# Kernel optimization log

Hardware: AMD Instinct MI355X
Metric: run time of the kernel (lower is better)

Reference implementation:

```python
import jax, jax.numpy as jnp
import numpy as np

B, N, DIM = 4, 2048, 512
HEADS, DIM_HEAD = 8, 64
HID = HEADS * DIM_HEAD


def setup_inputs() -> dict:
    key = jax.random.key(0)
    k1, k2, k3, k4, k5 = jax.random.split(key, 5)
    x = jax.random.normal(k1, (B, N, DIM), jnp.float32)
    pos_bias = jax.random.normal(k2, (HEADS, N, N), jnp.float32) * 0.02
    focus_present_mask = jax.random.bernoulli(k3, 0.5, (B,))
    w_qkv = jax.random.normal(k4, (DIM, 3 * HID), jnp.float32) * (DIM ** -0.5)
    w_out = jax.random.normal(k5, (HID, DIM), jnp.float32) * (HID ** -0.5)
    return {"x": x, "pos_bias": pos_bias, "focus_present_mask": focus_present_mask,
            "w_qkv": w_qkv, "w_out": w_out}


def reference(x, pos_bias, focus_present_mask, w_qkv, w_out):
    scale = DIM_HEAD ** -0.5
    qkv = x @ w_qkv                                   # (B, N, 3*HID)
    q, k, v = jnp.split(qkv, 3, axis=-1)

    def to_heads(t):  # (B, N, HID) -> (B, H, N, D)
        return t.reshape(B, N, HEADS, DIM_HEAD).transpose(0, 2, 1, 3)

    q = to_heads(q) * scale
    k = to_heads(k)
    v = to_heads(v)

    sim = jnp.einsum('bhid,bhjd->bhij', q, k) + pos_bias[None]  # (B, H, N, N)

    # focus_present_mask[b] True -> attend only to self (eye); False -> attend all
    eye = jnp.eye(N, dtype=bool)
    mask = jnp.where(focus_present_mask[:, None, None, None],
                     eye[None, None], jnp.bool_(True))          # (B,1,N,N)
    sim = jnp.where(mask, sim, -jnp.finfo(sim.dtype).max)

    attn = jax.nn.softmax(sim, axis=-1)  # stable softmax == subtract-max + softmax
    out = jnp.einsum('bhij,bhjd->bhid', attn, v)
    out = out.transpose(0, 2, 1, 3).reshape(B, N, HID)
    return out @ w_out
```

## Files before the change

kernel.cpp:

```cpp
#include <hip/hip_runtime.h>
#include <hip/hip_bf16.h>
#include <float.h>

#define B_   4
#define N_   2048
#define DIM_ 512
#define H_   8
#define DH_  64

typedef unsigned short ushort;
typedef __attribute__((ext_vector_type(8))) short short8;
typedef __attribute__((ext_vector_type(4))) float f32x4;

__device__ __forceinline__ ushort f2bf(float f) {
    union { float f; unsigned u; } v; v.f = f;
    return (ushort)((v.u + 0x7fffu + ((v.u >> 16) & 1u)) >> 16);
}
__device__ __forceinline__ float bf2f(ushort u) {
    union { unsigned u; float f; } v; v.u = ((unsigned)u) << 16;
    return v.f;
}

typedef const __attribute__((address_space(1))) unsigned int* gas_t;
typedef __attribute__((address_space(3))) unsigned int* las_t;
__device__ __forceinline__ void gl_lds16(const void* g, void* l) {
    __builtin_amdgcn_global_load_lds((gas_t)g, (las_t)l, 16, 0, 0);
}

__global__ __launch_bounds__(256) void prep_kernel(
    const float* __restrict__ x, const float* __restrict__ wqkv,
    const float* __restrict__ wo,
    ushort* __restrict__ xb, ushort* __restrict__ wqkvT, ushort* __restrict__ woT)
{
    __shared__ ushort tile[64][72];
    const int bx = blockIdx.x;
    const int t = threadIdx.x;
    if (bx < 2048) {
        int gid = bx * 256 + t;
        const float4* xv = (const float4*)x;
        float4 v0 = xv[gid * 2], v1 = xv[gid * 2 + 1];
        uint4 pk;
        pk.x = (unsigned)f2bf(v0.x) | ((unsigned)f2bf(v0.y) << 16);
        pk.y = (unsigned)f2bf(v0.z) | ((unsigned)f2bf(v0.w) << 16);
        pk.z = (unsigned)f2bf(v1.x) | ((unsigned)f2bf(v1.y) << 16);
        pk.w = (unsigned)f2bf(v1.z) | ((unsigned)f2bf(v1.w) << 16);
        ((uint4*)xb)[gid] = pk;
        return;
    }
    int bi = bx - 2048;
    const float* src; ushort* dst; int C, tc, tr;
    if (bi < 192) { src = wqkv; dst = wqkvT; C = 1536; tc = bi % 24; tr = bi / 24; }
    else { bi -= 192; src = wo; dst = woT; C = 512; tc = bi & 7; tr = bi >> 3; }

    const int row = t >> 2, c16 = (t & 3) * 16;
    const float* sp = src + (size_t)(tr * 64 + row) * C + tc * 64 + c16;
    #pragma unroll
    for (int i = 0; i < 4; ++i) {
        float4 v = ((const float4*)sp)[i];
        tile[row][c16 + i * 4 + 0] = f2bf(v.x);
        tile[row][c16 + i * 4 + 1] = f2bf(v.y);
        tile[row][c16 + i * 4 + 2] = f2bf(v.z);
        tile[row][c16 + i * 4 + 3] = f2bf(v.w);
    }
    __syncthreads();
    ushort s[16];
    #pragma unroll
    for (int i = 0; i < 16; ++i) s[i] = tile[c16 + i][row];
    ushort* dp = dst + (size_t)(tc * 64 + row) * 512 + tr * 64 + c16;
    *(uint4*)dp       = *(uint4*)&s[0];
    *(uint4*)(dp + 8) = *(uint4*)&s[8];
}

__global__ __launch_bounds__(256) void vtrans_kernel(
    const ushort* __restrict__ v, ushort* __restrict__ vT)
{
    __shared__ ushort tile[64][72];
    const int nt = blockIdx.x, bh = blockIdx.y;
    const int t = threadIdx.x;
    const int row = t >> 2, c16 = (t & 3) * 16;
    const ushort* src = v + ((size_t)bh * 2048 + nt * 64 + row) * 64 + c16;
    *(uint4*)&tile[row][c16]     = *(const uint4*)src;
    *(uint4*)&tile[row][c16 + 8] = *(const uint4*)(src + 8);
    __syncthreads();
    ushort s[16];
    #pragma unroll
    for (int i = 0; i < 16; ++i) s[i] = tile[c16 + i][row];
    ushort* dst = vT + ((size_t)bh * 64 + row) * 2048 + nt * 64 + c16;
    *(uint4*)dst       = *(uint4*)&s[0];
    *(uint4*)(dst + 8) = *(uint4*)&s[8];
}

__global__ __launch_bounds__(256) void qkv_gemm(
    const ushort* __restrict__ A, const ushort* __restrict__ Bt,
    ushort* __restrict__ qb, ushort* __restrict__ kb, ushort* __restrict__ vb)
{
    __shared__ ushort sA[128 * 64];
    __shared__ ushort sB[128 * 64];
    const int bn = blockIdx.x;
    const int bm = blockIdx.y;
    const int t = threadIdx.x, w_id = t >> 6, lane = t & 63;
    const int l15 = lane & 15, quad = lane >> 4;
    const int mo = (w_id & 1) * 64, no = (w_id >> 1) * 64;
    const int lr = lane >> 3, lc = (lane & 7) * 8;

    f32x4 acc[4][4] = {};

    for (int kt = 0; kt < 8; ++kt) {
        __syncthreads();
        #pragma unroll
        for (int i = 0; i < 4; ++i) {
            int j = w_id * 4 + i;
            gl_lds16(A  + (size_t)(bm * 128 + j * 8 + lr) * 512 + kt * 64 + lc, &sA[j * 512]);
            gl_lds16(Bt + (size_t)(bn * 128 + j * 8 + lr) * 512 + kt * 64 + lc, &sB[j * 512]);
        }
        __syncthreads();
        #pragma unroll
        for (int c = 0; c < 2; ++c) {
            short8 af[4], bf[4];
            #pragma unroll
            for (int mt = 0; mt < 4; ++mt)
                af[mt] = *(const short8*)&sA[(mo + mt * 16 + l15) * 64 + c * 32 + quad * 8];
            #pragma unroll
            for (int n2 = 0; n2 < 4; ++n2)
                bf[n2] = *(const short8*)&sB[(no + n2 * 16 + l15) * 64 + c * 32 + quad * 8];
            #pragma unroll
            for (int mt = 0; mt < 4; ++mt)
                #pragma unroll
                for (int n2 = 0; n2 < 4; ++n2)
                    acc[mt][n2] = __builtin_amdgcn_mfma_f32_16x16x32_bf16(af[mt], bf[n2], acc[mt][n2], 0, 0, 0);
        }
    }

    const int gn0 = bn * 128 + no;
    const int which = gn0 >> 9;
    const int h = (gn0 >> 6) & 7;
    ushort* dst = which == 0 ? qb : (which == 1 ? kb : vb);
    const float sc = which == 0 ? 0.125f : 1.0f;
    #pragma unroll
    for (int mt = 0; mt < 4; ++mt) {
        const int m0 = bm * 128 + mo + mt * 16 + quad * 4;
        #pragma unroll
        for (int n2 = 0; n2 < 4; ++n2) {
            int d = n2 * 16 + l15;
            #pragma unroll
            for (int r = 0; r < 4; ++r) {
                int m = m0 + r, b = m >> 11, n = m & 2047;
                dst[((size_t)(b * 8 + h) * 2048 + n) * 64 + d] = f2bf(acc[mt][n2][r] * sc);
            }
        }
    }
}

__global__ __launch_bounds__(256) void attn_kernel(
    const ushort* __restrict__ qg, const ushort* __restrict__ kg,
    const ushort* __restrict__ vTg, const float* __restrict__ bias,
    const int* __restrict__ mask,
    ushort* __restrict__ po, float* __restrict__ pl)
{
    const int bid = blockIdx.x;
    const int qblk = bid & 31, s = (bid >> 5) & 1, h = (bid >> 6) & 7, b = bid >> 9;
    if (mask[b] != 0) return;

    const int t = threadIdx.x, w_id = t >> 6, lane = t & 63;
    const int l15 = lane & 15, quad = lane >> 4;
    const int lr = lane >> 3, lc = (lane & 7) * 8;
    const int bh = b * 8 + h;
    const int kbase = s * 1024;

    __shared__ ushort lds_k[64 * 64];
    __shared__ ushort lds_vt[64 * 64];
    __shared__ ushort lds_sp[4 * 16 * 68];

    const ushort* kptr = kg  + (size_t)bh * 2048 * 64;
    const ushort* vtp  = vTg + (size_t)bh * 64 * 2048;

    const ushort* qrp = qg + (size_t)bh * 2048 * 64 + (size_t)(qblk * 64 + w_id * 16 + l15) * 64;
    short8 qf0 = *(const short8*)(qrp + quad * 8);
    short8 qf1 = *(const short8*)(qrp + 32 + quad * 8);

    const int qrow0 = qblk * 64 + w_id * 16 + quad * 4;
    const float* bp = bias + ((size_t)h * 2048 + qrow0) * 2048 + kbase;

    float breg[16];
    #pragma unroll
    for (int tt = 0; tt < 4; ++tt)
        #pragma unroll
        for (int r = 0; r < 4; ++r)
            breg[tt * 4 + r] = bp[(size_t)r * 2048 + tt * 16 + l15];

    f32x4 o[4] = {};
    float lsum[4] = {0.f, 0.f, 0.f, 0.f};

    for (int it = 0; it < 16; ++it) {
        __syncthreads();
        #pragma unroll
        for (int i = 0; i < 2; ++i) {
            int j = w_id * 2 + i;
            gl_lds16(kptr + (size_t)(kbase + it * 64 + j * 8 + lr) * 64 + lc, &lds_k[j * 512]);
            gl_lds16(vtp + (size_t)(j * 8 + lr) * 2048 + kbase + it * 64 + lc, &lds_vt[j * 512]);
        }
        __syncthreads();

        f32x4 sv[4] = {};
        #pragma unroll
        for (int tt = 0; tt < 4; ++tt) {
            short8 kf0 = *(const short8*)&lds_k[(tt * 16 + l15) * 64 + quad * 8];
            short8 kf1 = *(const short8*)&lds_k[(tt * 16 + l15) * 64 + 32 + quad * 8];
            sv[tt] = __builtin_amdgcn_mfma_f32_16x16x32_bf16(qf0, kf0, sv[tt], 0, 0, 0);
            sv[tt] = __builtin_amdgcn_mfma_f32_16x16x32_bf16(qf1, kf1, sv[tt], 0, 0, 0);
        }
        #pragma unroll
        for (int tt = 0; tt < 4; ++tt)
            #pragma unroll
            for (int r = 0; r < 4; ++r)
                sv[tt][r] += breg[tt * 4 + r];

        if (it < 15) {
            #pragma unroll
            for (int tt = 0; tt < 4; ++tt)
                #pragma unroll
                for (int r = 0; r < 4; ++r)
                    breg[tt * 4 + r] = bp[(size_t)r * 2048 + (it + 1) * 64 + tt * 16 + l15];
        }

        const int prow0 = (w_id * 16 + quad * 4) * 68;
        #pragma unroll
        for (int r = 0; r < 4; ++r) {
            float e0 = __expf(sv[0][r]), e1 = __expf(sv[1][r]);
            float e2 = __expf(sv[2][r]), e3 = __expf(sv[3][r]);
            lsum[r] += (e0 + e1) + (e2 + e3);
            const int pr = prow0 + r * 68;
            lds_sp[pr + l15]      = f2bf(e0);
            lds_sp[pr + 16 + l15] = f2bf(e1);
            lds_sp[pr + 32 + l15] = f2bf(e2);
            lds_sp[pr + 48 + l15] = f2bf(e3);
        }

        asm volatile("s_waitcnt lgkmcnt(0)" ::: "memory");

        short8 pf0 = *(const short8*)&lds_sp[(w_id * 16 + l15) * 68 + quad * 8];
        short8 pf1 = *(const short8*)&lds_sp[(w_id * 16 + l15) * 68 + 32 + quad * 8];
        #pragma unroll
        for (int nt = 0; nt < 4; ++nt) {
            short8 vf0 = *(const short8*)&lds_vt[(nt * 16 + l15) * 64 + quad * 8];
            short8 vf1 = *(const short8*)&lds_vt[(nt * 16 + l15) * 64 + 32 + quad * 8];
            o[nt] = __builtin_amdgcn_mfma_f32_16x16x32_bf16(pf0, vf0, o[nt], 0, 0, 0);
            o[nt] = __builtin_amdgcn_mfma_f32_16x16x32_bf16(pf1, vf1, o[nt], 0, 0, 0);
        }
    }

    #pragma unroll
    for (int r = 0; r < 4; ++r) {
        #pragma unroll
        for (int off = 1; off < 16; off <<= 1)
            lsum[r] += __shfl_xor(lsum[r], off, 64);
    }

    #pragma unroll
    for (int r = 0; r < 4; ++r) {
        const int qrow = qrow0 + r;
        const size_t base = ((size_t)(s * 32 + bh) * 2048 + qrow) * 64;
        #pragma unroll
        for (int nt = 0; nt < 4; ++nt)
            po[base + nt * 16 + l15] = f2bf(o[nt][r]);
        if (l15 == 0)
            pl[(size_t)(s * 32 + bh) * 2048 + qrow] = lsum[r];
    }
}

__global__ __launch_bounds__(256) void combine_kernel(
    const ushort* __restrict__ po, const float* __restrict__ pl,
    const ushort* __restrict__ vb, const int* __restrict__ mask,
    ushort* __restrict__ ob)
{
    const int gid = blockIdx.x * 256 + threadIdx.x;
    const int dd = (gid & 7) * 8;
    const int h = (gid >> 3) & 7, n = (gid >> 6) & 2047, b = gid >> 17;
    const int bh = b * 8 + h;
    ushort* op = ob + ((size_t)b * 2048 + n) * 512 + h * 64 + dd;
    if (mask[b] != 0) {
        *(uint4*)op = *(const uint4*)(vb + ((size_t)bh * 2048 + n) * 64 + dd);
        return;
    }
    const size_t i1 = (size_t)bh * 2048 + n;
    const size_t i2 = (size_t)(32 + bh) * 2048 + n;
    float inv = 1.f / (pl[i1] + pl[i2]);
    uint4 ua = *(const uint4*)(po + i1 * 64 + dd);
    uint4 ub = *(const uint4*)(po + i2 * 64 + dd);
    const ushort* pa = (const ushort*)&ua;
    const ushort* pb = (const ushort*)&ub;
    ushort res[8];
    #pragma unroll
    for (int j = 0; j < 8; ++j)
        res[j] = f2bf((bf2f(pa[j]) + bf2f(pb[j])) * inv);
    *(uint4*)op = *(uint4*)res;
}

__global__ __launch_bounds__(256) void out_gemm(
    const ushort* __restrict__ A, const ushort* __restrict__ Bt,
    float* __restrict__ out)
{
    __shared__ ushort sA[128 * 64];
    __shared__ ushort sB[128 * 64];
    const int bn = blockIdx.x;
    const int bm = blockIdx.y;
    const int t = threadIdx.x, w_id = t >> 6, lane = t & 63;
    const int l15 = lane & 15, quad = lane >> 4;
    const int mo = (w_id & 1) * 64, no = (w_id >> 1) * 64;
    const int lr = lane >> 3, lc = (lane & 7) * 8;

    f32x4 acc[4][4] = {};

    for (int kt = 0; kt < 8; ++kt) {
        __syncthreads();
        #pragma unroll
        for (int i = 0; i < 4; ++i) {
            int j = w_id * 4 + i;
            gl_lds16(A  + (size_t)(bm * 128 + j * 8 + lr) * 512 + kt * 64 + lc, &sA[j * 512]);
            gl_lds16(Bt + (size_t)(bn * 128 + j * 8 + lr) * 512 + kt * 64 + lc, &sB[j * 512]);
        }
        __syncthreads();
        #pragma unroll
        for (int c = 0; c < 2; ++c) {
            short8 af[4], bf[4];
            #pragma unroll
            for (int mt = 0; mt < 4; ++mt)
                af[mt] = *(const short8*)&sA[(mo + mt * 16 + l15) * 64 + c * 32 + quad * 8];
            #pragma unroll
            for (int n2 = 0; n2 < 4; ++n2)
                bf[n2] = *(const short8*)&sB[(no + n2 * 16 + l15) * 64 + c * 32 + quad * 8];
            #pragma unroll
            for (int mt = 0; mt < 4; ++mt)
                #pragma unroll
                for (int n2 = 0; n2 < 4; ++n2)
                    acc[mt][n2] = __builtin_amdgcn_mfma_f32_16x16x32_bf16(af[mt], bf[n2], acc[mt][n2], 0, 0, 0);
        }
    }
    #pragma unroll
    for (int mt = 0; mt < 4; ++mt) {
        const int m0 = bm * 128 + mo + mt * 16 + quad * 4;
        #pragma unroll
        for (int n2 = 0; n2 < 4; ++n2) {
            int col = bn * 128 + no + n2 * 16 + l15;
            #pragma unroll
            for (int r = 0; r < 4; ++r)
                out[(size_t)(m0 + r) * 512 + col] = acc[mt][n2][r];
        }
    }
}

extern "C" void kernel_launch(void* const* d_in, const int* in_sizes, int n_in,
                              void* d_out, int out_size, void* d_ws, size_t ws_size,
                              hipStream_t stream)
{
    const float* x        = (const float*)d_in[0];
    const float* pos_bias = (const float*)d_in[1];
    const int*   mask     = (const int*)d_in[2];
    const float* w_qkv    = (const float*)d_in[3];
    const float* w_out    = (const float*)d_in[4];
    float* out = (float*)d_out;

    char* ws = (char*)d_ws;
    ushort* qb    = (ushort*)(ws + 0);
    ushort* kb    = (ushort*)(ws + 8388608);
    ushort* vb    = (ushort*)(ws + 16777216);
    ushort* vT    = (ushort*)(ws + 25165824);
    ushort* xb    = (ushort*)(ws + 33554432);
    ushort* ob    = (ushort*)(ws + 33554432);
    ushort* po    = (ushort*)(ws + 41943040);
    float*  pl    = (float* )(ws + 58720256);
    ushort* woT   = (ushort*)(ws + 59244544);
    ushort* wqkvT = (ushort*)(ws + 59768832);

    prep_kernel<<<2304, 256, 0, stream>>>(x, w_qkv, w_out, xb, wqkvT, woT);
    qkv_gemm<<<dim3(12, 64), 256, 0, stream>>>(xb, wqkvT, qb, kb, vb);
    vtrans_kernel<<<dim3(32, 32), 256, 0, stream>>>(vb, vT);
    attn_kernel<<<2048, 256, 0, stream>>>(qb, kb, vT, pos_bias, mask, po, pl);
    combine_kernel<<<2048, 256, 0, stream>>>(po, pl, vb, mask, ob);
    out_gemm<<<dim3(4, 64), 256, 0, stream>>>(ob, woT, out);
}
```

Before: 299.8 us.

## Fuse x conversion and V transpose into QKV GEMM, read K/V directly in attention

Converts x from fp32 to bf16 inside the QKV GEMM's A-tile load, and writes the transposed V directly from the GEMM epilogue. This removes the separate x conversion pass and the vtrans kernel. The attention kernel drops its LDS staging of K and V^T and loads MFMA fragments straight from global memory, which removes two block barriers per iteration but relies on cache for reuse across waves. It also stores P with truncating bf16 conversion and pads the P tile stride to 72.

```diff
diff --git a/kernel.cpp b/kernel.cpp
--- a/kernel.cpp
+++ b/kernel.cpp
@@ -16,6 +16,10 @@
     union { float f; unsigned u; } v; v.f = f;
     return (ushort)((v.u + 0x7fffu + ((v.u >> 16) & 1u)) >> 16);
 }
+__device__ __forceinline__ ushort f2bf_t(float f) {
+    union { float f; unsigned u; } v; v.f = f;
+    return (ushort)(v.u >> 16);
+}
 __device__ __forceinline__ float bf2f(ushort u) {
     union { unsigned u; float f; } v; v.u = ((unsigned)u) << 16;
     return v.f;
@@ -28,26 +32,12 @@
 }
 
 __global__ __launch_bounds__(256) void prep_kernel(
-    const float* __restrict__ x, const float* __restrict__ wqkv,
-    const float* __restrict__ wo,
-    ushort* __restrict__ xb, ushort* __restrict__ wqkvT, ushort* __restrict__ woT)
+    const float* __restrict__ wqkv, const float* __restrict__ wo,
+    ushort* __restrict__ wqkvT, ushort* __restrict__ woT)
 {
     __shared__ ushort tile[64][72];
-    const int bx = blockIdx.x;
+    int bi = blockIdx.x;
     const int t = threadIdx.x;
-    if (bx < 2048) {
-        int gid = bx * 256 + t;
-        const float4* xv = (const float4*)x;
-        float4 v0 = xv[gid * 2], v1 = xv[gid * 2 + 1];
-        uint4 pk;
-        pk.x = (unsigned)f2bf(v0.x) | ((unsigned)f2bf(v0.y) << 16);
-        pk.y = (unsigned)f2bf(v0.z) | ((unsigned)f2bf(v0.w) << 16);
-        pk.z = (unsigned)f2bf(v1.x) | ((unsigned)f2bf(v1.y) << 16);
-        pk.w = (unsigned)f2bf(v1.z) | ((unsigned)f2bf(v1.w) << 16);
-        ((uint4*)xb)[gid] = pk;
-        return;
-    }
-    int bi = bx - 2048;
     const float* src; ushort* dst; int C, tc, tr;
     if (bi < 192) { src = wqkv; dst = wqkvT; C = 1536; tc = bi % 24; tr = bi / 24; }
     else { bi -= 192; src = wo; dst = woT; C = 512; tc = bi & 7; tr = bi >> 3; }
@@ -71,28 +61,219 @@
     *(uint4*)(dp + 8) = *(uint4*)&s[8];
 }
 
-__global__ __launch_bounds__(256) void vtrans_kernel(
-    const ushort* __restrict__ v, ushort* __restrict__ vT)
-{
-    __shared__ ushort tile[64][72];
-    const int nt = blockIdx.x, bh = blockIdx.y;
-    const int t = threadIdx.x;
-    const int row = t >> 2, c16 = (t & 3) * 16;
-    const ushort* src = v + ((size_t)bh * 2048 + nt * 64 + row) * 64 + c16;
-    *(uint4*)&tile[row][c16]     = *(const uint4*)src;
-    *(uint4*)&tile[row][c16 + 8] = *(const uint4*)(src + 8);
-    __syncthreads();
-    ushort s[16];
-    #pragma unroll
-    for (int i = 0; i < 16; ++i) s[i] = tile[c16 + i][row];
-    ushort* dst = vT + ((size_t)bh * 64 + row) * 2048 + nt * 64 + c16;
-    *(uint4*)dst       = *(uint4*)&s[0];
-    *(uint4*)(dst + 8) = *(uint4*)&s[8];
-}
-
 __global__ __launch_bounds__(256) void qkv_gemm(
+    const float* __restrict__ X, const ushort* __restrict__ Bt,
+    ushort* __restrict__ qb, ushort* __restrict__ kb, ushort* __restrict__ vb,
+    ushort* __restrict__ vT)
+{
+    __shared__ ushort sA[128 * 72];
+    __shared__ ushort sB[128 * 64];
+    const int bn = blockIdx.x;
+    const int bm = blockIdx.y;
+    const int t = threadIdx.x, w_id = t >> 6, lane = t & 63;
+    const int l15 = lane & 15, quad = lane >> 4;
+    const int mo = (w_id & 1) * 64, no = (w_id >> 1) * 64;
+    const int lr = lane >> 3, lc = (lane & 7) * 8;
+
+    f32x4 acc[4][4] = {};
+
+    for (int kt = 0; kt < 8; ++kt) {
+        __syncthreads();
+        #pragma unroll
+        for (int i = 0; i < 4; ++i) {
+            int j = w_id * 4 + i;
+            gl_lds16(Bt + (size_t)(bn * 128 + j * 8 + lr) * 512 + kt * 64 + lc, &sB[j * 512]);
+        }
+        #pragma unroll
+        for (int j2 = 0; j2 < 8; ++j2) {
+            int f = j2 * 1024 + t * 4;
+            int row = f >> 6, col = f & 63;
+            float4 xv = *(const float4*)(X + (size_t)(bm * 128 + row) * 512 + kt * 64 + col);
+            uint2 pk;
+            pk.x = (unsigned)f2bf(xv.x) | ((unsigned)f2bf(xv.y) << 16);
+            pk.y = (unsigned)f2bf(xv.z) | ((unsigned)f2bf(xv.w) << 16);
+            *(uint2*)&sA[row * 72 + col] = pk;
+        }
+        __syncthreads();
+        #pragma unroll
+        for (int c = 0; c < 2; ++c) {
+            short8 af[4], bf[4];
+            #pragma unroll
+            for (int mt = 0; mt < 4; ++mt)
+                af[mt] = *(const short8*)&sA[(mo + mt * 16 + l15) * 72 + c * 32 + quad * 8];
+            #pragma unroll
+            for (int n2 = 0; n2 < 4; ++n2)
+                bf[n2] = *(const short8*)&sB[(no + n2 * 16 + l15) * 64 + c * 32 + quad * 8];
+            #pragma unroll
+            for (int mt = 0; mt < 4; ++mt)
+                #pragma unroll
+                for (int n2 = 0; n2 < 4; ++n2)
+                    acc[mt][n2] = __builtin_amdgcn_mfma_f32_16x16x32_bf16(af[mt], bf[n2], acc[mt][n2], 0, 0, 0);
+        }
+    }
+
+    const int gn0 = bn * 128 + no;
+    const int which = gn0 >> 9;
+    const int h = (gn0 >> 6) & 7;
+    ushort* dst = which == 0 ? qb : (which == 1 ? kb : vb);
+    const float sc = which == 0 ? 0.125f : 1.0f;
+    #pragma unroll
+    for (int mt = 0; mt < 4; ++mt) {
+        const int m0 = bm * 128 + mo + mt * 16 + quad * 4;
+        const int b = m0 >> 11, n = m0 & 2047;
+        #pragma unroll
+        for (int n2 = 0; n2 < 4; ++n2) {
+            int d = n2 * 16 + l15;
+            #pragma unroll
+            for (int r = 0; r < 4; ++r)
+                dst[((size_t)(b * 8 + h) * 2048 + n + r) * 64 + d] = f2bf(acc[mt][n2][r] * sc);
+            if (which == 2) {
+                uint2 pk;
+                pk.x = (unsigned)f2bf(acc[mt][n2][0]) | ((unsigned)f2bf(acc[mt][n2][1]) << 16);
+                pk.y = (unsigned)f2bf(acc[mt][n2][2]) | ((unsigned)f2bf(acc[mt][n2][3]) << 16);
+                *(uint2*)(vT + ((size_t)(b * 8 + h) * 64 + d) * 2048 + n) = pk;
+            }
+        }
+    }
+}
+
+__global__ __launch_bounds__(256) void attn_kernel(
+    const ushort* __restrict__ qg, const ushort* __restrict__ kg,
+    const ushort* __restrict__ vTg, const float* __restrict__ bias,
+    const int* __restrict__ mask,
+    ushort* __restrict__ po, float* __restrict__ pl)
+{
+    const int bid = blockIdx.x;
+    const int qblk = bid & 31, s = (bid >> 5) & 1, h = (bid >> 6) & 7, b = bid >> 9;
+    if (mask[b] != 0) return;
+
+    const int t = threadIdx.x, w_id = t >> 6, lane = t & 63;
+    const int l15 = lane & 15, quad = lane >> 4;
+    const int bh = b * 8 + h;
+    const int kbase = s * 1024;
+
+    __shared__ ushort lds_sp[4 * 16 * 72];
+
+    const ushort* kp = kg  + ((size_t)bh * 2048 + kbase) * 64;
+    const ushort* vp = vTg + (size_t)bh * 64 * 2048 + kbase;
+
+    const ushort* qrp = qg + (size_t)bh * 2048 * 64 + (size_t)(qblk * 64 + w_id * 16 + l15) * 64;
+    short8 qf0 = *(const short8*)(qrp + quad * 8);
+    short8 qf1 = *(const short8*)(qrp + 32 + quad * 8);
+
+    const int qrow0 = qblk * 64 + w_id * 16 + quad * 4;
+    const float* bp = bias + ((size_t)h * 2048 + qrow0) * 2048 + kbase;
+
+    float breg[16];
+    #pragma unroll
+    for (int tt = 0; tt < 4; ++tt)
+        #pragma unroll
+        for (int r = 0; r < 4; ++r)
+            breg[tt * 4 + r] = bp[(size_t)r * 2048 + tt * 16 + l15];
+
+    f32x4 o[4] = {};
+    float lsum[4] = {0.f, 0.f, 0.f, 0.f};
+
+    for (int it = 0; it < 16; ++it) {
+        const ushort* kit = kp + it * 64 * 64;
+
+        f32x4 sv[4] = {};
+        #pragma unroll
+        for (int tt = 0; tt < 4; ++tt) {
+            short8 kf0 = *(const short8*)(kit + (tt * 16 + l15) * 64 + quad * 8);
+            short8 kf1 = *(const short8*)(kit + (tt * 16 + l15) * 64 + 32 + quad * 8);
+            sv[tt] = __builtin_amdgcn_mfma_f32_16x16x32_bf16(qf0, kf0, sv[tt], 0, 0, 0);
+            sv[tt] = __builtin_amdgcn_mfma_f32_16x16x32_bf16(qf1, kf1, sv[tt], 0, 0, 0);
+        }
+        #pragma unroll
+        for (int tt = 0; tt < 4; ++tt)
+            #pragma unroll
+            for (int r = 0; r < 4; ++r)
+                sv[tt][r] += breg[tt * 4 + r];
+
+        if (it < 15) {
+            #pragma unroll
+            for (int tt = 0; tt < 4; ++tt)
+                #pragma unroll
+                for (int r = 0; r < 4; ++r)
+                    breg[tt * 4 + r] = bp[(size_t)r * 2048 + (it + 1) * 64 + tt * 16 + l15];
+        }
+
+        #pragma unroll
+        for (int r = 0; r < 4; ++r) {
+            float e0 = __expf(sv[0][r]), e1 = __expf(sv[1][r]);
+            float e2 = __expf(sv[2][r]), e3 = __expf(sv[3][r]);
+            lsum[r] += (e0 + e1) + (e2 + e3);
+            const int pr = (w_id * 16 + quad * 4 + r) * 72;
+            lds_sp[pr + l15]      = f2bf_t(e0);
+            lds_sp[pr + 16 + l15] = f2bf_t(e1);
+            lds_sp[pr + 32 + l15] = f2bf_t(e2);
+            lds_sp[pr + 48 + l15] = f2bf_t(e3);
+        }
+
+        asm volatile("s_waitcnt lgkmcnt(0)" ::: "memory");
+
+        short8 pf0 = *(const short8*)&lds_sp[(w_id * 16 + l15) * 72 + quad * 8];
+        short8 pf1 = *(const short8*)&lds_sp[(w_id * 16 + l15) * 72 + 32 + quad * 8];
+        #pragma unroll
+        for (int nt = 0; nt < 4; ++nt) {
+            short8 vf0 = *(const short8*)(vp + (size_t)(nt * 16 + l15) * 2048 + it * 64 + quad * 8);
+            short8 vf1 = *(const short8*)(vp + (size_t)(nt * 16 + l15) * 2048 + it * 64 + 32 + quad * 8);
+            o[nt] = __builtin_amdgcn_mfma_f32_16x16x32_bf16(pf0, vf0, o[nt], 0, 0, 0);
+            o[nt] = __builtin_amdgcn_mfma_f32_16x16x32_bf16(pf1, vf1, o[nt], 0, 0, 0);
+        }
+    }
+
+    #pragma unroll
+    for (int r = 0; r < 4; ++r) {
+        #pragma unroll
+        for (int off = 1; off < 16; off <<= 1)
+            lsum[r] += __shfl_xor(lsum[r], off, 64);
+    }
+
+    #pragma unroll
+    for (int r = 0; r < 4; ++r) {
+        const int qrow = qrow0 + r;
+        const size_t base = ((size_t)(s * 32 + bh) * 2048 + qrow) * 64;
+        #pragma unroll
+        for (int nt = 0; nt < 4; ++nt)
+            po[base + nt * 16 + l15] = f2bf(o[nt][r]);
+        if (l15 == 0)
+            pl[(size_t)(s * 32 + bh) * 2048 + qrow] = lsum[r];
+    }
+}
+
+__global__ __launch_bounds__(256) void combine_kernel(
+    const ushort* __restrict__ po, const float* __restrict__ pl,
+    const ushort* __restrict__ vb, const int* __restrict__ mask,
+    ushort* __restrict__ ob)
+{
+    const int gid = blockIdx.x * 256 + threadIdx.x;
+    const int dd = (gid & 7) * 8;
+    const int h = (gid >> 3) & 7, n = (gid >> 6) & 2047, b = gid >> 17;
+    const int bh = b * 8 + h;
+    ushort* op = ob + ((size_t)b * 2048 + n) * 512 + h * 64 + dd;
+    if (mask[b] != 0) {
+        *(uint4*)op = *(const uint4*)(vb + ((size_t)bh * 2048 + n) * 64 + dd);
+        return;
+    }
+    const size_t i1 = (size_t)bh * 2048 + n;
+    const size_t i2 = (size_t)(32 + bh) * 2048 + n;
+    float inv = 1.f / (pl[i1] + pl[i2]);
+    uint4 ua = *(const uint4*)(po + i1 * 64 + dd);
+    uint4 ub = *(const uint4*)(po + i2 * 64 + dd);
+    const ushort* pa = (const ushort*)&ua;
+    const ushort* pb = (const ushort*)&ub;
+    ushort res[8];
+    #pragma unroll
+    for (int j = 0; j < 8; ++j)
+        res[j] = f2bf((bf2f(pa[j]) + bf2f(pb[j])) * inv);
+    *(uint4*)op = *(uint4*)res;
+}
+
+__global__ __launch_bounds__(256) void out_gemm(
     const ushort* __restrict__ A, const ushort* __restrict__ Bt,
-    ushort* __restrict__ qb, ushort* __restrict__ kb, ushort* __restrict__ vb)
+    float* __restrict__ out)
 {
     __shared__ ushort sA[128 * 64];
     __shared__ ushort sB[128 * 64];
@@ -130,212 +311,6 @@
                     acc[mt][n2] = __builtin_amdgcn_mfma_f32_16x16x32_bf16(af[mt], bf[n2], acc[mt][n2], 0, 0, 0);
         }
     }
-
-    const int gn0 = bn * 128 + no;
-    const int which = gn0 >> 9;
-    const int h = (gn0 >> 6) & 7;
-    ushort* dst = which == 0 ? qb : (which == 1 ? kb : vb);
-    const float sc = which == 0 ? 0.125f : 1.0f;
-    #pragma unroll
-    for (int mt = 0; mt < 4; ++mt) {
-        const int m0 = bm * 128 + mo + mt * 16 + quad * 4;
-        #pragma unroll
-        for (int n2 = 0; n2 < 4; ++n2) {
-            int d = n2 * 16 + l15;
-            #pragma unroll
-            for (int r = 0; r < 4; ++r) {
-                int m = m0 + r, b = m >> 11, n = m & 2047;
-                dst[((size_t)(b * 8 + h) * 2048 + n) * 64 + d] = f2bf(acc[mt][n2][r] * sc);
-            }
-        }
-    }
-}
-
-__global__ __launch_bounds__(256) void attn_kernel(
-    const ushort* __restrict__ qg, const ushort* __restrict__ kg,
-    const ushort* __restrict__ vTg, const float* __restrict__ bias,
-    const int* __restrict__ mask,
-    ushort* __restrict__ po, float* __restrict__ pl)
-{
-    const int bid = blockIdx.x;
-    const int qblk = bid & 31, s = (bid >> 5) & 1, h = (bid >> 6) & 7, b = bid >> 9;
-    if (mask[b] != 0) return;
-
-    const int t = threadIdx.x, w_id = t >> 6, lane = t & 63;
-    const int l15 = lane & 15, quad = lane >> 4;
-    const int lr = lane >> 3, lc = (lane & 7) * 8;
-    const int bh = b * 8 + h;
-    const int kbase = s * 1024;
-
-    __shared__ ushort lds_k[64 * 64];
-    __shared__ ushort lds_vt[64 * 64];
-    __shared__ ushort lds_sp[4 * 16 * 68];
-
-    const ushort* kptr = kg  + (size_t)bh * 2048 * 64;
-    const ushort* vtp  = vTg + (size_t)bh * 64 * 2048;
-
-    const ushort* qrp = qg + (size_t)bh * 2048 * 64 + (size_t)(qblk * 64 + w_id * 16 + l15) * 64;
-    short8 qf0 = *(const short8*)(qrp + quad * 8);
-    short8 qf1 = *(const short8*)(qrp + 32 + quad * 8);
-
-    const int qrow0 = qblk * 64 + w_id * 16 + quad * 4;
-    const float* bp = bias + ((size_t)h * 2048 + qrow0) * 2048 + kbase;
-
-    float breg[16];
-    #pragma unroll
-    for (int tt = 0; tt < 4; ++tt)
-        #pragma unroll
-        for (int r = 0; r < 4; ++r)
-            breg[tt * 4 + r] = bp[(size_t)r * 2048 + tt * 16 + l15];
-
-    f32x4 o[4] = {};
-    float lsum[4] = {0.f, 0.f, 0.f, 0.f};
-
-    for (int it = 0; it < 16; ++it) {
-        __syncthreads();
-        #pragma unroll
-        for (int i = 0; i < 2; ++i) {
-            int j = w_id * 2 + i;
-            gl_lds16(kptr + (size_t)(kbase + it * 64 + j * 8 + lr) * 64 + lc, &lds_k[j * 512]);
-            gl_lds16(vtp + (size_t)(j * 8 + lr) * 2048 + kbase + it * 64 + lc, &lds_vt[j * 512]);
-        }
-        __syncthreads();
-
-        f32x4 sv[4] = {};
-        #pragma unroll
-        for (int tt = 0; tt < 4; ++tt) {
-            short8 kf0 = *(const short8*)&lds_k[(tt * 16 + l15) * 64 + quad * 8];
-            short8 kf1 = *(const short8*)&lds_k[(tt * 16 + l15) * 64 + 32 + quad * 8];
-            sv[tt] = __builtin_amdgcn_mfma_f32_16x16x32_bf16(qf0, kf0, sv[tt], 0, 0, 0);
-            sv[tt] = __builtin_amdgcn_mfma_f32_16x16x32_bf16(qf1, kf1, sv[tt], 0, 0, 0);
-        }
-        #pragma unroll
-        for (int tt = 0; tt < 4; ++tt)
-            #pragma unroll
-            for (int r = 0; r < 4; ++r)
-                sv[tt][r] += breg[tt * 4 + r];
-
-        if (it < 15) {
-            #pragma unroll
-            for (int tt = 0; tt < 4; ++tt)
-                #pragma unroll
-                for (int r = 0; r < 4; ++r)
-                    breg[tt * 4 + r] = bp[(size_t)r * 2048 + (it + 1) * 64 + tt * 16 + l15];
-        }
-
-        const int prow0 = (w_id * 16 + quad * 4) * 68;
-        #pragma unroll
-        for (int r = 0; r < 4; ++r) {
-            float e0 = __expf(sv[0][r]), e1 = __expf(sv[1][r]);
-            float e2 = __expf(sv[2][r]), e3 = __expf(sv[3][r]);
-            lsum[r] += (e0 + e1) + (e2 + e3);
-            const int pr = prow0 + r * 68;
-            lds_sp[pr + l15]      = f2bf(e0);
-            lds_sp[pr + 16 + l15] = f2bf(e1);
-            lds_sp[pr + 32 + l15] = f2bf(e2);
-            lds_sp[pr + 48 + l15] = f2bf(e3);
-        }
-
-        asm volatile("s_waitcnt lgkmcnt(0)" ::: "memory");
-
-        short8 pf0 = *(const short8*)&lds_sp[(w_id * 16 + l15) * 68 + quad * 8];
-        short8 pf1 = *(const short8*)&lds_sp[(w_id * 16 + l15) * 68 + 32 + quad * 8];
-        #pragma unroll
-        for (int nt = 0; nt < 4; ++nt) {
-            short8 vf0 = *(const short8*)&lds_vt[(nt * 16 + l15) * 64 + quad * 8];
-            short8 vf1 = *(const short8*)&lds_vt[(nt * 16 + l15) * 64 + 32 + quad * 8];
-            o[nt] = __builtin_amdgcn_mfma_f32_16x16x32_bf16(pf0, vf0, o[nt], 0, 0, 0);
-            o[nt] = __builtin_amdgcn_mfma_f32_16x16x32_bf16(pf1, vf1, o[nt], 0, 0, 0);
-        }
-    }
-
-    #pragma unroll
-    for (int r = 0; r < 4; ++r) {
-        #pragma unroll
-        for (int off = 1; off < 16; off <<= 1)
-            lsum[r] += __shfl_xor(lsum[r], off, 64);
-    }
-
-    #pragma unroll
-    for (int r = 0; r < 4; ++r) {
-        const int qrow = qrow0 + r;
-        const size_t base = ((size_t)(s * 32 + bh) * 2048 + qrow) * 64;
-        #pragma unroll
-        for (int nt = 0; nt < 4; ++nt)
-            po[base + nt * 16 + l15] = f2bf(o[nt][r]);
-        if (l15 == 0)
-            pl[(size_t)(s * 32 + bh) * 2048 + qrow] = lsum[r];
-    }
-}
-
-__global__ __launch_bounds__(256) void combine_kernel(
-    const ushort* __restrict__ po, const float* __restrict__ pl,
-    const ushort* __restrict__ vb, const int* __restrict__ mask,
-    ushort* __restrict__ ob)
-{
-    const int gid = blockIdx.x * 256 + threadIdx.x;
-    const int dd = (gid & 7) * 8;
-    const int h = (gid >> 3) & 7, n = (gid >> 6) & 2047, b = gid >> 17;
-    const int bh = b * 8 + h;
-    ushort* op = ob + ((size_t)b * 2048 + n) * 512 + h * 64 + dd;
-    if (mask[b] != 0) {
-        *(uint4*)op = *(const uint4*)(vb + ((size_t)bh * 2048 + n) * 64 + dd);
-        return;
-    }
-    const size_t i1 = (size_t)bh * 2048 + n;
-    const size_t i2 = (size_t)(32 + bh) * 2048 + n;
-    float inv = 1.f / (pl[i1] + pl[i2]);
-    uint4 ua = *(const uint4*)(po + i1 * 64 + dd);
-    uint4 ub = *(const uint4*)(po + i2 * 64 + dd);
-    const ushort* pa = (const ushort*)&ua;
-    const ushort* pb = (const ushort*)&ub;
-    ushort res[8];
-    #pragma unroll
-    for (int j = 0; j < 8; ++j)
-        res[j] = f2bf((bf2f(pa[j]) + bf2f(pb[j])) * inv);
-    *(uint4*)op = *(uint4*)res;
-}
-
-__global__ __launch_bounds__(256) void out_gemm(
-    const ushort* __restrict__ A, const ushort* __restrict__ Bt,
-    float* __restrict__ out)
-{
-    __shared__ ushort sA[128 * 64];
-    __shared__ ushort sB[128 * 64];
-    const int bn = blockIdx.x;
-    const int bm = blockIdx.y;
-    const int t = threadIdx.x, w_id = t >> 6, lane = t & 63;
-    const int l15 = lane & 15, quad = lane >> 4;
-    const int mo = (w_id & 1) * 64, no = (w_id >> 1) * 64;
-    const int lr = lane >> 3, lc = (lane & 7) * 8;
-
-    f32x4 acc[4][4] = {};
-
-    for (int kt = 0; kt < 8; ++kt) {
-        __syncthreads();
-        #pragma unroll
-        for (int i = 0; i < 4; ++i) {
-            int j = w_id * 4 + i;
-            gl_lds16(A  + (size_t)(bm * 128 + j * 8 + lr) * 512 + kt * 64 + lc, &sA[j * 512]);
-            gl_lds16(Bt + (size_t)(bn * 128 + j * 8 + lr) * 512 + kt * 64 + lc, &sB[j * 512]);
-        }
-        __syncthreads();
-        #pragma unroll
-        for (int c = 0; c < 2; ++c) {
-            short8 af[4], bf[4];
-            #pragma unroll
-            for (int mt = 0; mt < 4; ++mt)
-                af[mt] = *(const short8*)&sA[(mo + mt * 16 + l15) * 64 + c * 32 + quad * 8];
-            #pragma unroll
-            for (int n2 = 0; n2 < 4; ++n2)
-                bf[n2] = *(const short8*)&sB[(no + n2 * 16 + l15) * 64 + c * 32 + quad * 8];
-            #pragma unroll
-            for (int mt = 0; mt < 4; ++mt)
-                #pragma unroll
-                for (int n2 = 0; n2 < 4; ++n2)
-                    acc[mt][n2] = __builtin_amdgcn_mfma_f32_16x16x32_bf16(af[mt], bf[n2], acc[mt][n2], 0, 0, 0);
-        }
-    }
     #pragma unroll
     for (int mt = 0; mt < 4; ++mt) {
         const int m0 = bm * 128 + mo + mt * 16 + quad * 4;
@@ -365,16 +340,14 @@
     ushort* kb    = (ushort*)(ws + 8388608);
     ushort* vb    = (ushort*)(ws + 16777216);
     ushort* vT    = (ushort*)(ws + 25165824);
-    ushort* xb    = (ushort*)(ws + 33554432);
     ushort* ob    = (ushort*)(ws + 33554432);
     ushort* po    = (ushort*)(ws + 41943040);
     float*  pl    = (float* )(ws + 58720256);
     ushort* woT   = (ushort*)(ws + 59244544);
     ushort* wqkvT = (ushort*)(ws + 59768832);
 
-    prep_kernel<<<2304, 256, 0, stream>>>(x, w_qkv, w_out, xb, wqkvT, woT);
-    qkv_gemm<<<dim3(12, 64), 256, 0, stream>>>(xb, wqkvT, qb, kb, vb);
-    vtrans_kernel<<<dim3(32, 32), 256, 0, stream>>>(vb, vT);
+    prep_kernel<<<256, 256, 0, stream>>>(w_qkv, w_out, wqkvT, woT);
+    qkv_gemm<<<dim3(12, 64), 256, 0, stream>>>(x, wqkvT, qb, kb, vb, vT);
     attn_kernel<<<2048, 256, 0, stream>>>(qb, kb, vT, pos_bias, mask, po, pl);
     combine_kernel<<<2048, 256, 0, stream>>>(po, pl, vb, mask, ob);
     out_gemm<<<dim3(4, 64), 256, 0, stream>>>(ob, woT, out);
```

Result: slower. 363.3 us (+21.2%).
